# Kernel tuning notes

Measured on AMD Instinct MI355X. Metric: run time of the kernel, lower is better.

Reference implementation:

```python
import jax, jax.numpy as jnp
import numpy as np

B, N, C = 8, 4096, 3
IN_DIM = 2
HID = 512
NL = 256          # num_latents
DEPTH = 6
H, DH = 8, 64     # heads, dim_head (cross and latent)
INNER = H * DH
LAT = 32          # latent (bottleneck) dim
NF, MAXF = 12, 4  # NeRF num_freq, max_freq_log2
FF = 4 * HID
SCALE = DH ** -0.5
NERF_DIM = 2 * NF * IN_DIM  # 48


def layer_norm(x, g, b, eps=1e-5):
    m = jnp.mean(x, axis=-1, keepdims=True)
    v = jnp.mean((x - m) ** 2, axis=-1, keepdims=True)
    return (x - m) * jax.lax.rsqrt(v + eps) * g + b


def nerf_encode(pos):
    # log-sampled frequency bands: 2^linspace(0, MAXF, NF)
    freqs = 2.0 ** jnp.linspace(0.0, float(MAXF), NF)
    ang = pos[..., None] * freqs            # [B,N,IN_DIM,NF]
    enc = jnp.concatenate([jnp.sin(ang), jnp.cos(ang)], axis=-1)  # [B,N,IN_DIM,2NF]
    return enc.reshape(*pos.shape[:-1], NERF_DIM)


def mha(q, k, v):
    # q:[B,Nq,INNER] k,v:[B,Nk,INNER] -> [B,Nq,INNER]
    def split(t):
        b, n, _ = t.shape
        return t.reshape(b, n, H, DH).transpose(0, 2, 1, 3)  # [B,H,n,DH]
    qh, kh, vh = split(q), split(k), split(v)
    sim = jnp.einsum('bhid,bhjd->bhij', qh, kh) * SCALE
    attn = jax.nn.softmax(sim, axis=-1)
    o = jnp.einsum('bhij,bhjd->bhid', attn, vh)
    return o.transpose(0, 2, 1, 3).reshape(q.shape[0], q.shape[1], INNER)


def setup_inputs():
    key = jax.random.key(0)
    ks = iter(jax.random.split(key, 64))
    def w(*shape):
        return jax.random.normal(next(ks), shape, jnp.float32) * 0.02
    inp = {}
    inp['x'] = jax.random.normal(next(ks), (B, N, C), jnp.float32)
    inp['pos'] = jax.random.uniform(next(ks), (B, N, IN_DIM), jnp.float32)
    # input embeddings
    inp['W_pos'] = w(NERF_DIM, HID); inp['b_pos'] = jnp.zeros((HID,), jnp.float32)
    inp['W_in'] = w(C, HID); inp['b_in'] = jnp.zeros((HID,), jnp.float32)
    inp['latents'] = w(NL, HID)
    # cross-attention (PreNormCross: norm on q, k, v)
    for n in ('lnq', 'lnk', 'lnv'):
        inp[n + '_g'] = jnp.ones((HID,), jnp.float32)
        inp[n + '_b'] = jnp.zeros((HID,), jnp.float32)
    inp['cWq'] = w(HID, INNER); inp['cWk'] = w(HID, INNER); inp['cWv'] = w(HID, INNER)
    inp['cWo'] = w(INNER, HID); inp['c_bo'] = jnp.zeros((HID,), jnp.float32)
    # self-attention + FFN stacks
    inp['ln1_g'] = jnp.ones((DEPTH, HID), jnp.float32); inp['ln1_b'] = jnp.zeros((DEPTH, HID), jnp.float32)
    inp['sWq'] = w(DEPTH, HID, INNER); inp['sWkv'] = w(DEPTH, HID, 2 * INNER)
    inp['sWo'] = w(DEPTH, INNER, HID); inp['s_bo'] = jnp.zeros((DEPTH, HID), jnp.float32)
    inp['ln2_g'] = jnp.ones((DEPTH, HID), jnp.float32); inp['ln2_b'] = jnp.zeros((DEPTH, HID), jnp.float32)
    inp['fW1'] = w(DEPTH, HID, FF); inp['f_b1'] = jnp.zeros((DEPTH, FF), jnp.float32)
    inp['fW2'] = w(DEPTH, FF, HID); inp['f_b2'] = jnp.zeros((DEPTH, HID), jnp.float32)
    # final norm + gaussian bottleneck projection (mean, logvar)
    inp['lnf_g'] = jnp.ones((HID,), jnp.float32); inp['lnf_b'] = jnp.zeros((HID,), jnp.float32)
    inp['Wb'] = w(HID, 2 * LAT); inp['bb'] = jnp.zeros((2 * LAT,), jnp.float32)
    return inp


def reference(x, pos, W_pos, b_pos, W_in, b_in, latents,
              lnq_g, lnq_b, lnk_g, lnk_b, lnv_g, lnv_b,
              cWq, cWk, cWv, cWo, c_bo,
              ln1_g, ln1_b, sWq, sWkv, sWo, s_bo,
              ln2_g, ln2_b, fW1, f_b1, fW2, f_b2,
              lnf_g, lnf_b, Wb, bb):
    # positional embedding (FourierPositionalEmbedding with relu)
    kin = jax.nn.relu(nerf_encode(pos) @ W_pos + b_pos)   # [B,N,HID]
    vin = x @ W_in + b_in                                 # [B,N,HID]
    vin = vin + kin                                       # include_pos_in_value
    lat = jnp.broadcast_to(latents, (B, NL, HID))
    # cross-attention block (PreNormCross + residual)
    qn = layer_norm(lat, lnq_g, lnq_b)
    kn = layer_norm(kin, lnk_g, lnk_b)
    vn = layer_norm(vin, lnv_g, lnv_b)
    o = mha(qn @ cWq, kn @ cWk, vn @ cWv) @ cWo + c_bo
    lat = lat + o
    # latent self-attention + FFN blocks
    for i in range(DEPTH):
        h1 = layer_norm(lat, ln1_g[i], ln1_b[i])
        q = h1 @ sWq[i]
        k, v = jnp.split(h1 @ sWkv[i], 2, axis=-1)
        lat = lat + (mha(q, k, v) @ sWo[i] + s_bo[i])
        h2 = layer_norm(lat, ln2_g[i], ln2_b[i])
        lat = lat + (jax.nn.gelu(h2 @ fW1[i] + f_b1[i]) @ fW2[i] + f_b2[i])
    # bottleneck projection -> (mean | logvar)
    out = layer_norm(lat, lnf_g, lnf_b) @ Wb + bb         # [B,NL,2*LAT]
    return out
```

## Files before the change

### kernel.cpp

```cpp
#include <hip/hip_runtime.h>
#include <hip/hip_bf16.h>

#define DEV __device__ __forceinline__

typedef __attribute__((ext_vector_type(8))) short short8;
typedef __attribute__((ext_vector_type(4))) float floatx4;

DEV short f2bf(float f) {
  unsigned u = __float_as_uint(f);
  u += 0x7fffu + ((u >> 16) & 1u);
  return (short)(u >> 16);
}
DEV float bf2f(short s) {
  return __uint_as_float(((unsigned)(unsigned short)s) << 16);
}
DEV float wred(float v) {
#pragma unroll
  for (int m = 1; m < 64; m <<= 1) v += __shfl_xor(v, m);
  return v;
}
DEV floatx4 mfma16(short8 a, short8 b, floatx4 c) {
  return __builtin_amdgcn_mfma_f32_16x16x32_bf16(a, b, c, 0, 0, 0);
}
DEV void gload16(void* lds, const void* g) {
  __builtin_amdgcn_global_load_lds(
      (const __attribute__((address_space(1))) unsigned int*)g,
      (__attribute__((address_space(3))) unsigned int*)lds, 16, 0, 0);
}

struct MatDesc { const float* src; int K; int N; int kp; int off; };
struct MatTable { MatDesc m[36]; };

__global__ __launch_bounds__(256) void wtrans_kernel(MatTable T, short* __restrict__ dst) {
  int mi = blockIdx.y;
  MatDesc d = T.m[mi];
  int tilesx = d.N >> 5, tilesy = d.kp >> 5;
  int tb = blockIdx.x;
  if (tb >= tilesx * tilesy) return;
  int ty = tb / tilesx, tx = tb % tilesx;
  __shared__ float tile[32][33];
  int tid = threadIdx.x;
#pragma unroll
  for (int i = 0; i < 4; ++i) {
    int e = tid + i * 256, lr = e >> 5, lc = e & 31;
    int kk = ty * 32 + lr;
    tile[lr][lc] = (kk < d.K) ? d.src[(size_t)kk * d.N + tx * 32 + lc] : 0.f;
  }
  __syncthreads();
#pragma unroll
  for (int i = 0; i < 4; ++i) {
    int e = tid + i * 256, lr = e >> 5, lc = e & 31;
    dst[(size_t)d.off + (size_t)(tx * 32 + lr) * d.kp + ty * 32 + lc] = f2bf(tile[lc][lr]);
  }
}

__global__ __launch_bounds__(256) void enc_kernel(const float* __restrict__ pos,
                                                  short* __restrict__ enc) {
  int idx = blockIdx.x * 256 + threadIdx.x;
  int row = idx >> 3, oct = idx & 7;
  float p0 = pos[row * 2], p1 = pos[row * 2 + 1];
  short8 o;
#pragma unroll
  for (int j = 0; j < 8; ++j) {
    int k = oct * 8 + j;
    float val = 0.f;
    if (k < 48) {
      int dd = k / 24, rem = k % 24;
      int trig = rem / 12, f = rem % 12;
      float ang = (dd ? p1 : p0) * exp2f((4.0f / 11.0f) * (float)f);
      val = trig ? __cosf(ang) : __sinf(ang);
    }
    o[j] = f2bf(val);
  }
  *(short8*)&enc[(size_t)row * 64 + oct * 8] = o;
}

__global__ __launch_bounds__(512) void embed2_kernel(
    const short* __restrict__ enc, const short* __restrict__ Wt,
    const float* __restrict__ b_pos, const float* __restrict__ W_in,
    const float* __restrict__ b_in, const float* __restrict__ x,
    const float* __restrict__ lnk_g, const float* __restrict__ lnk_b,
    const float* __restrict__ lnv_g, const float* __restrict__ lnv_b,
    short* __restrict__ kn, short* __restrict__ vn) {
  __shared__ short Wl[512 * 64];
  __shared__ short El[128 * 64];
  int tid = threadIdx.x;
  int lane = tid & 63, wv = tid >> 6;
  int c = lane & 15, g = lane >> 4;
  int blk = blockIdx.x * 128;
#pragma unroll
  for (int gi = 0; gi < 8; ++gi) {
    int grp = wv * 8 + gi;
    int row = grp * 8 + (lane >> 3), kc = lane & 7;
    gload16(&Wl[grp * 512], &Wt[(size_t)row * 64 + ((kc ^ (row & 7)) * 8)]);
  }
#pragma unroll
  for (int gi = 0; gi < 2; ++gi) {
    int grp = wv * 2 + gi;
    int row = grp * 8 + (lane >> 3), kc = lane & 7;
    gload16(&El[grp * 512], &enc[(size_t)(blk + row) * 64 + ((kc ^ (row & 7)) * 8)]);
  }
  __syncthreads();

  floatx4 acc[32];
  floatx4 zf = {0.f, 0.f, 0.f, 0.f};
#pragma unroll
  for (int nf = 0; nf < 32; ++nf) acc[nf] = zf;
  short8 af[2];
#pragma unroll
  for (int ks = 0; ks < 2; ++ks)
    af[ks] = *(const short8*)&El[(wv * 16 + c) * 64 + ((ks * 4 + g) ^ (c & 7)) * 8];
#pragma unroll
  for (int nf = 0; nf < 32; ++nf) {
#pragma unroll
    for (int ks = 0; ks < 2; ++ks) {
      short8 bf8 = *(const short8*)&Wl[(nf * 16 + c) * 64 + ((ks * 4 + g) ^ (c & 7)) * 8];
      acc[nf] = mfma16(af[ks], bf8, acc[nf]);
    }
  }

  int rowbase = blk + wv * 16 + g * 4;
  float x0[4], x1[4], x2[4];
  float s1[4], q1[4], s2[4], q2[4];
#pragma unroll
  for (int r = 0; r < 4; ++r) {
    x0[r] = x[(size_t)(rowbase + r) * 3];
    x1[r] = x[(size_t)(rowbase + r) * 3 + 1];
    x2[r] = x[(size_t)(rowbase + r) * 3 + 2];
    s1[r] = 0; q1[r] = 0; s2[r] = 0; q2[r] = 0;
  }
#pragma unroll
  for (int nf = 0; nf < 32; ++nf) {
    int col = nf * 16 + c;
    float bp = b_pos[col];
    float w0 = W_in[col], w1 = W_in[512 + col], w2 = W_in[1024 + col], bi = b_in[col];
#pragma unroll
    for (int r = 0; r < 4; ++r) {
      float kk = fmaxf(acc[nf][r] + bp, 0.f);
      float vv = kk + x0[r] * w0 + x1[r] * w1 + x2[r] * w2 + bi;
      acc[nf][r] = kk;
      s1[r] += kk; q1[r] += kk * kk; s2[r] += vv; q2[r] += vv * vv;
    }
  }
  float m1[4], r1[4], m2[4], r2[4];
#pragma unroll
  for (int r = 0; r < 4; ++r) {
#pragma unroll
    for (int msk = 1; msk < 16; msk <<= 1) {
      s1[r] += __shfl_xor(s1[r], msk); q1[r] += __shfl_xor(q1[r], msk);
      s2[r] += __shfl_xor(s2[r], msk); q2[r] += __shfl_xor(q2[r], msk);
    }
    m1[r] = s1[r] * (1.f / 512.f);
    r1[r] = rsqrtf(q1[r] * (1.f / 512.f) - m1[r] * m1[r] + 1e-5f);
    m2[r] = s2[r] * (1.f / 512.f);
    r2[r] = rsqrtf(q2[r] * (1.f / 512.f) - m2[r] * m2[r] + 1e-5f);
  }
#pragma unroll
  for (int nf = 0; nf < 32; ++nf) {
    int col = nf * 16 + c;
    float w0 = W_in[col], w1 = W_in[512 + col], w2 = W_in[1024 + col], bi = b_in[col];
    float gk = lnk_g[col], bk = lnk_b[col], gv = lnv_g[col], bv = lnv_b[col];
#pragma unroll
    for (int r = 0; r < 4; ++r) {
      float kk = acc[nf][r];
      float vv = kk + x0[r] * w0 + x1[r] * w1 + x2[r] * w2 + bi;
      size_t idx = (size_t)(rowbase + r) * 512 + col;
      kn[idx] = f2bf((kk - m1[r]) * r1[r] * gk + bk);
      vn[idx] = f2bf((vv - m2[r]) * r2[r] * gv + bv);
    }
  }
}

__global__ __launch_bounds__(256) void ln_kernel(
    const float* __restrict__ in, const float* __restrict__ g,
    const float* __restrict__ b, short* __restrict__ out, int M) {
  int row = blockIdx.x * 4 + (threadIdx.x >> 6);
  if (row >= M) return;
  int lane = threadIdx.x & 63;
  float v[8]; float s = 0, q = 0;
#pragma unroll
  for (int j = 0; j < 8; ++j) {
    v[j] = in[(size_t)row * 512 + lane + 64 * j];
    s += v[j]; q += v[j] * v[j];
  }
  s = wred(s); q = wred(q);
  float m = s * (1.f / 512.f);
  float rs = rsqrtf(q * (1.f / 512.f) - m * m + 1e-5f);
#pragma unroll
  for (int j = 0; j < 8; ++j) {
    int cc = lane + 64 * j;
    out[(size_t)row * 512 + cc] = f2bf((v[j] - m) * rs * g[cc] + b[cc]);
  }
}

__global__ void bcast_kernel(const float* __restrict__ latents, float* __restrict__ lat) {
  int i = blockIdx.x * 256 + threadIdx.x;
  lat[i] = latents[i & 131071];
}

template <int EPI>
DEV void epi_store(void* outp, size_t idx, float xv) {
  if (EPI == 0) {
    ((short*)outp)[idx] = f2bf(xv);
  } else if (EPI == 1) {
    float t = 0.7978845608f * (xv + 0.044715f * xv * xv * xv);
    ((short*)outp)[idx] = f2bf(0.5f * xv * (1.f + tanhf(t)));
  } else if (EPI == 2) {
    ((float*)outp)[idx] += xv;
  } else {
    ((float*)outp)[idx] = xv;
  }
}

template <int EPI>
__global__ __launch_bounds__(256) void gemm_kernel(
    const short* __restrict__ A, const short* __restrict__ Wt,
    const float* __restrict__ bias, void* __restrict__ outp,
    int M, int N, int K, int ldo) {
  __shared__ short Alds[128 * 64];
  __shared__ short Blds[128 * 64];
  int tid = threadIdx.x;
  int brow = blockIdx.y * 128, bcol = blockIdx.x * 128;
  int lane = tid & 63, wvid = tid >> 6;
  int wr = wvid >> 1, wc = wvid & 1;
  int g = lane >> 4, c = lane & 15;
  floatx4 zf = {0.f, 0.f, 0.f, 0.f};
  floatx4 acc[4][4];
#pragma unroll
  for (int i = 0; i < 4; ++i)
#pragma unroll
    for (int j = 0; j < 4; ++j) acc[i][j] = zf;

  int srow = (lane >> 3), skc = lane & 7;
  for (int k0 = 0; k0 < K; k0 += 64) {
#pragma unroll
    for (int gi = 0; gi < 4; ++gi) {
      int grp = wvid * 4 + gi;
      int row = grp * 8 + srow;
      int sw = ((skc ^ (row & 7)) * 8);
      gload16(&Alds[grp * 512], &A[(size_t)(brow + row) * K + k0 + sw]);
      gload16(&Blds[grp * 512], &Wt[(size_t)(bcol + row) * K + k0 + sw]);
    }
    __syncthreads();
#pragma unroll
    for (int ks = 0; ks < 2; ++ks) {
      int slot = ((ks * 4 + g) ^ (c & 7)) * 8;
      short8 af[4], bf8[4];
#pragma unroll
      for (int mf = 0; mf < 4; ++mf)
        af[mf] = *(const short8*)&Alds[(wr * 64 + mf * 16 + c) * 64 + slot];
#pragma unroll
      for (int nf = 0; nf < 4; ++nf)
        bf8[nf] = *(const short8*)&Blds[(wc * 64 + nf * 16 + c) * 64 + slot];
#pragma unroll
      for (int mf = 0; mf < 4; ++mf)
#pragma unroll
        for (int nf = 0; nf < 4; ++nf)
          acc[mf][nf] = mfma16(af[mf], bf8[nf], acc[mf][nf]);
    }
    __syncthreads();
  }

#pragma unroll
  for (int mf = 0; mf < 4; ++mf) {
#pragma unroll
    for (int nf = 0; nf < 4; ++nf) {
      int col = bcol + wc * 64 + nf * 16 + c;
      float bv = bias ? bias[col] : 0.f;
      int row0 = brow + wr * 64 + mf * 16 + g * 4;
#pragma unroll
      for (int r = 0; r < 4; ++r)
        epi_store<EPI>(outp, (size_t)(row0 + r) * ldo + col, acc[mf][nf][r] + bv);
    }
  }
}

template <int EPI>
__global__ __launch_bounds__(256) void gemm64_kernel(
    const short* __restrict__ A, const short* __restrict__ Wt,
    const float* __restrict__ bias, void* __restrict__ outp,
    int M, int N, int K, int ldo) {
  __shared__ short Alds[64 * 64];
  __shared__ short Blds[64 * 64];
  int tid = threadIdx.x;
  int brow = blockIdx.y * 64, bcol = blockIdx.x * 64;
  int lane = tid & 63, wvid = tid >> 6;
  int wr = wvid >> 1, wc = wvid & 1;
  int g = lane >> 4, c = lane & 15;
  floatx4 zf = {0.f, 0.f, 0.f, 0.f};
  floatx4 acc[2][2];
#pragma unroll
  for (int i = 0; i < 2; ++i)
#pragma unroll
    for (int j = 0; j < 2; ++j) acc[i][j] = zf;

  int srow = (lane >> 3), skc = lane & 7;
  for (int k0 = 0; k0 < K; k0 += 64) {
#pragma unroll
    for (int gi = 0; gi < 2; ++gi) {
      int grp = wvid * 2 + gi;
      int row = grp * 8 + srow;
      int sw = ((skc ^ (row & 7)) * 8);
      gload16(&Alds[grp * 512], &A[(size_t)(brow + row) * K + k0 + sw]);
      gload16(&Blds[grp * 512], &Wt[(size_t)(bcol + row) * K + k0 + sw]);
    }
    __syncthreads();
#pragma unroll
    for (int ks = 0; ks < 2; ++ks) {
      int slot = ((ks * 4 + g) ^ (c & 7)) * 8;
      short8 af[2], bf8[2];
#pragma unroll
      for (int mf = 0; mf < 2; ++mf)
        af[mf] = *(const short8*)&Alds[(wr * 32 + mf * 16 + c) * 64 + slot];
#pragma unroll
      for (int nf = 0; nf < 2; ++nf)
        bf8[nf] = *(const short8*)&Blds[(wc * 32 + nf * 16 + c) * 64 + slot];
#pragma unroll
      for (int mf = 0; mf < 2; ++mf)
#pragma unroll
        for (int nf = 0; nf < 2; ++nf)
          acc[mf][nf] = mfma16(af[mf], bf8[nf], acc[mf][nf]);
    }
    __syncthreads();
  }

#pragma unroll
  for (int mf = 0; mf < 2; ++mf) {
#pragma unroll
    for (int nf = 0; nf < 2; ++nf) {
      int col = bcol + wc * 32 + nf * 16 + c;
      float bv = bias ? bias[col] : 0.f;
      int row0 = brow + wr * 32 + mf * 16 + g * 4;
#pragma unroll
      for (int r = 0; r < 4; ++r)
        epi_store<EPI>(outp, (size_t)(row0 + r) * ldo + col, acc[mf][nf][r] + bv);
    }
  }
}

__global__ __launch_bounds__(256) void flash_kernel(
    const short* __restrict__ q, const short* __restrict__ k,
    const short* __restrict__ v, short* __restrict__ out,
    int qrs, int qbrows, long kvbstride, int kvrstride, int nkv) {
  __shared__ short Qs[64 * 64];
  __shared__ short Ks[64 * 64];
  __shared__ short Vt[64 * 72];
  __shared__ short Ps[64 * 72];
  int tid = threadIdx.x;
  int b = blockIdx.z, h = blockIdx.y, qt = blockIdx.x;
  int lane = tid & 63, wv = tid >> 6;
  int g = lane >> 4, c = lane & 15;
  int srow = lane >> 3, skc = lane & 7;

#pragma unroll
  for (int gi = 0; gi < 2; ++gi) {
    int grp = wv * 2 + gi;
    int row = grp * 8 + srow;
    int sw = ((skc ^ (row & 7)) * 8);
    gload16(&Qs[grp * 512],
            &q[((size_t)(b * qbrows) + qt * 64 + row) * qrs + h * 64 + sw]);
  }

  float m_[4], l_[4];
  floatx4 zf = {0.f, 0.f, 0.f, 0.f};
  floatx4 o_[4];
#pragma unroll
  for (int r = 0; r < 4; ++r) { m_[r] = -3.0e38f; l_[r] = 0.f; }
#pragma unroll
  for (int f = 0; f < 4; ++f) o_[f] = zf;

  for (int t0 = 0; t0 < nkv; t0 += 64) {
#pragma unroll
    for (int gi = 0; gi < 2; ++gi) {
      int grp = wv * 2 + gi;
      int row = grp * 8 + srow;
      int sw = ((skc ^ (row & 7)) * 8);
      gload16(&Ks[grp * 512],
              &k[(size_t)b * kvbstride + (size_t)(t0 + row) * kvrstride + h * 64 + sw]);
    }
#pragma unroll
    for (int it = 0; it < 2; ++it) {
      int ch = tid + it * 256;
      int j = ch >> 3, f0 = (ch & 7) * 8, mm = ch & 7, tg = j >> 3;
      short8 tv = *(const short8*)&v[(size_t)b * kvbstride + (size_t)(t0 + j) * kvrstride + h * 64 + f0];
#pragma unroll
      for (int jj = 0; jj < 8; ++jj)
        Vt[(f0 + jj) * 72 + ((tg ^ mm) * 8) + (j & 7)] = tv[jj];
    }
    __syncthreads();

    floatx4 s[4];
#pragma unroll
    for (int f = 0; f < 4; ++f) s[f] = zf;
#pragma unroll
    for (int ks = 0; ks < 2; ++ks) {
      int slot = ((ks * 4 + g) ^ (c & 7)) * 8;
      short8 a = *(const short8*)&Qs[(wv * 16 + c) * 64 + slot];
#pragma unroll
      for (int f = 0; f < 4; ++f) {
        short8 b8 = *(const short8*)&Ks[(f * 16 + c) * 64 + slot];
        s[f] = mfma16(a, b8, s[f]);
      }
    }
#pragma unroll
    for (int f = 0; f < 4; ++f)
#pragma unroll
      for (int r = 0; r < 4; ++r) s[f][r] *= 0.125f;

    float nm[4], sf[4], rs[4];
#pragma unroll
    for (int r = 0; r < 4; ++r) {
      float t = fmaxf(fmaxf(s[0][r], s[1][r]), fmaxf(s[2][r], s[3][r]));
#pragma unroll
      for (int msk = 1; msk < 16; msk <<= 1) t = fmaxf(t, __shfl_xor(t, msk));
      nm[r] = fmaxf(m_[r], t);
      sf[r] = __expf(m_[r] - nm[r]);
      rs[r] = 0.f;
    }
#pragma unroll
    for (int f = 0; f < 4; ++f)
#pragma unroll
      for (int r = 0; r < 4; ++r) {
        float p = __expf(s[f][r] - nm[r]);
        s[f][r] = p; rs[r] += p;
      }
#pragma unroll
    for (int r = 0; r < 4; ++r) {
#pragma unroll
      for (int msk = 1; msk < 16; msk <<= 1) rs[r] += __shfl_xor(rs[r], msk);
      l_[r] = l_[r] * sf[r] + rs[r];
      m_[r] = nm[r];
    }
#pragma unroll
    for (int f = 0; f < 4; ++f)
#pragma unroll
      for (int r = 0; r < 4; ++r) o_[f][r] *= sf[r];
#pragma unroll
    for (int f = 0; f < 4; ++f)
#pragma unroll
      for (int r = 0; r < 4; ++r)
        Ps[(wv * 16 + g * 4 + r) * 72 + f * 16 + c] = f2bf(s[f][r]);
    __syncthreads();
#pragma unroll
    for (int ks = 0; ks < 2; ++ks) {
      short8 pa = *(const short8*)&Ps[(wv * 16 + c) * 72 + ks * 32 + g * 8];
#pragma unroll
      for (int f = 0; f < 4; ++f) {
        int mm = (2 * f + (c >> 3)) & 7;
        short8 vb = *(const short8*)&Vt[(f * 16 + c) * 72 + ((ks * 4 + g) ^ mm) * 8];
        o_[f] = mfma16(pa, vb, o_[f]);
      }
    }
    __syncthreads();
  }

#pragma unroll
  for (int f = 0; f < 4; ++f)
#pragma unroll
    for (int r = 0; r < 4; ++r) {
      int row = qt * 64 + wv * 16 + g * 4 + r;
      float val = o_[f][r] / l_[r];
      out[((size_t)(b * 256 + row)) * 512 + h * 64 + f * 16 + c] = f2bf(val);
    }
}

extern "C" void kernel_launch(void* const* d_in, const int* in_sizes, int n_in,
                              void* d_out, int out_size, void* d_ws, size_t ws_size,
                              hipStream_t stream) {
  const float* x       = (const float*)d_in[0];
  const float* pos     = (const float*)d_in[1];
  const float* W_pos   = (const float*)d_in[2];
  const float* b_pos   = (const float*)d_in[3];
  const float* W_in    = (const float*)d_in[4];
  const float* b_in    = (const float*)d_in[5];
  const float* latents = (const float*)d_in[6];
  const float* lnq_g   = (const float*)d_in[7];
  const float* lnq_b   = (const float*)d_in[8];
  const float* lnk_g   = (const float*)d_in[9];
  const float* lnk_b   = (const float*)d_in[10];
  const float* lnv_g   = (const float*)d_in[11];
  const float* lnv_b   = (const float*)d_in[12];
  const float* cWq     = (const float*)d_in[13];
  const float* cWk     = (const float*)d_in[14];
  const float* cWv     = (const float*)d_in[15];
  const float* cWo     = (const float*)d_in[16];
  const float* c_bo    = (const float*)d_in[17];
  const float* ln1_g   = (const float*)d_in[18];
  const float* ln1_b   = (const float*)d_in[19];
  const float* sWq     = (const float*)d_in[20];
  const float* sWkv    = (const float*)d_in[21];
  const float* sWo     = (const float*)d_in[22];
  const float* s_bo    = (const float*)d_in[23];
  const float* ln2_g   = (const float*)d_in[24];
  const float* ln2_b   = (const float*)d_in[25];
  const float* fW1     = (const float*)d_in[26];
  const float* f_b1    = (const float*)d_in[27];
  const float* fW2     = (const float*)d_in[28];
  const float* f_b2    = (const float*)d_in[29];
  const float* lnf_g   = (const float*)d_in[30];
  const float* lnf_b   = (const float*)d_in[31];
  const float* Wb      = (const float*)d_in[32];
  const float* bbv     = (const float*)d_in[33];
  float* outp = (float*)d_out;

  size_t W = 0;
  size_t o_cWq = W; W += 512 * 512;
  size_t o_cWk = W; W += 512 * 512;
  size_t o_cWv = W; W += 512 * 512;
  size_t o_cWo = W; W += 512 * 512;
  size_t o_Wb  = W; W += 64 * 512;
  size_t o_Wpos = W; W += 512 * 64;
  size_t o_sQKV[6], o_sWo[6], o_fW1[6], o_fW2[6];
  for (int i = 0; i < 6; ++i) {
    o_sQKV[i] = W; W += 1536 * 512;
    o_sWo[i]  = W; W += 512 * 512;
    o_fW1[i]  = W; W += 2048 * 512;
    o_fW2[i]  = W; W += 512 * 2048;
  }
  MatTable T;
  int nm = 0;
  auto add = [&](const float* s, int K, int N, int kp, size_t off) {
    T.m[nm].src = s; T.m[nm].K = K; T.m[nm].N = N; T.m[nm].kp = kp;
    T.m[nm].off = (int)off; ++nm;
  };
  add(cWq, 512, 512, 512, o_cWq); add(cWk, 512, 512, 512, o_cWk);
  add(cWv, 512, 512, 512, o_cWv); add(cWo, 512, 512, 512, o_cWo);
  add(Wb, 512, 64, 512, o_Wb);
  add(W_pos, 48, 512, 64, o_Wpos);
  for (int i = 0; i < 6; ++i) {
    add(sWq  + (size_t)i * 512 * 512,  512, 512,  512, o_sQKV[i]);
    add(sWkv + (size_t)i * 512 * 1024, 512, 1024, 512, o_sQKV[i] + 512 * 512);
    add(sWo  + (size_t)i * 512 * 512,  512, 512,  512, o_sWo[i]);
    add(fW1  + (size_t)i * 512 * 2048, 512, 2048, 512, o_fW1[i]);
    add(fW2  + (size_t)i * 2048 * 512, 2048, 512, 2048, o_fW2[i]);
  }

  char* p = (char*)d_ws;
  auto carve = [&](size_t bytes) {
    char* r = p; p += (bytes + 255) & ~(size_t)255; return r;
  };
  short* wtb   = (short*)carve(W * 2);
  short* enc   = (short*)carve((size_t)32768 * 64 * 2);
  short* kn    = (short*)carve(33554432);
  short* vn    = (short*)carve(33554432);
  short* kvc   = (short*)carve((size_t)32768 * 1024 * 2);
  short* latn0 = (short*)carve(262144);
  short* qc    = (short*)carve(262144);
  float* lat   = (float*)carve(4194304);
  short* attno = kn;
  short* h     = vn;
  short* qkv   = (short*)((char*)vn + 2097152);
  short* ffh   = (short*)((char*)vn + 8388608);

  wtrans_kernel<<<dim3(1024, 36), 256, 0, stream>>>(T, wtb);
  enc_kernel<<<1024, 256, 0, stream>>>(pos, enc);
  embed2_kernel<<<256, 512, 0, stream>>>(enc, wtb + o_Wpos, b_pos, W_in, b_in, x,
                                         lnk_g, lnk_b, lnv_g, lnv_b, kn, vn);
  bcast_kernel<<<4096, 256, 0, stream>>>(latents, lat);
  ln_kernel<<<64, 256, 0, stream>>>(latents, lnq_g, lnq_b, latn0, 256);
  gemm64_kernel<0><<<dim3(8, 4), 256, 0, stream>>>(latn0, wtb + o_cWq, nullptr, qc, 256, 512, 512, 512);
  gemm_kernel<0><<<dim3(4, 256), 256, 0, stream>>>(kn, wtb + o_cWk, nullptr, kvc, 32768, 512, 512, 1024);
  gemm_kernel<0><<<dim3(4, 256), 256, 0, stream>>>(vn, wtb + o_cWv, nullptr, kvc + 512, 32768, 512, 512, 1024);
  flash_kernel<<<dim3(4, 8, 8), 256, 0, stream>>>(qc, kvc, kvc + 512, attno,
                                                  512, 0, (long)4096 * 1024, 1024, 4096);
  gemm64_kernel<2><<<dim3(8, 32), 256, 0, stream>>>(attno, wtb + o_cWo, c_bo, lat, 2048, 512, 512, 512);

  for (int i = 0; i < 6; ++i) {
    ln_kernel<<<512, 256, 0, stream>>>(lat, ln1_g + i * 512, ln1_b + i * 512, h, 2048);
    gemm64_kernel<0><<<dim3(24, 32), 256, 0, stream>>>(h, wtb + o_sQKV[i], nullptr, qkv, 2048, 1536, 512, 1536);
    flash_kernel<<<dim3(4, 8, 8), 256, 0, stream>>>(qkv, qkv + 512, qkv + 1024, attno,
                                                    1536, 256, (long)256 * 1536, 1536, 256);
    gemm64_kernel<2><<<dim3(8, 32), 256, 0, stream>>>(attno, wtb + o_sWo[i], s_bo + i * 512, lat, 2048, 512, 512, 512);
    ln_kernel<<<512, 256, 0, stream>>>(lat, ln2_g + i * 512, ln2_b + i * 512, h, 2048);
    gemm_kernel<1><<<dim3(16, 16), 256, 0, stream>>>(h, wtb + o_fW1[i], f_b1 + i * 2048, ffh, 2048, 2048, 512, 2048);
    gemm64_kernel<2><<<dim3(8, 32), 256, 0, stream>>>(ffh, wtb + o_fW2[i], f_b2 + i * 512, lat, 2048, 512, 2048, 512);
  }
  ln_kernel<<<512, 256, 0, stream>>>(lat, lnf_g, lnf_b, h, 2048);
  gemm64_kernel<3><<<dim3(1, 32), 256, 0, stream>>>(h, wtb + o_Wb, bbv, outp, 2048, 64, 512, 64);
}
```

Measured before the change: 888.8 us.

## Split attention over KV segments with a combine kernel; interleave kn/vn buffers

Replaces the single-pass flash attention with a split-KV variant that writes per-segment partial outputs, row maxima and sums, followed by a combine kernel that rescales and merges them. Cross-attention uses 8 segments and self-attention uses 2, raising grid size from 256 blocks to 2048/512 so more CUs are occupied. Also interleaves kn/vn into one row-strided buffer (adding an lda parameter to the GEMMs) and switches the FFN up-projection to the 64-tile GEMM. The cost is extra fp32 partial traffic and an additional kernel launch per attention.

```diff
diff --git a/kernel.cpp b/kernel.cpp
--- a/kernel.cpp
+++ b/kernel.cpp
@@ -81,7 +81,7 @@
     const float* __restrict__ b_in, const float* __restrict__ x,
     const float* __restrict__ lnk_g, const float* __restrict__ lnk_b,
     const float* __restrict__ lnv_g, const float* __restrict__ lnv_b,
-    short* __restrict__ kn, short* __restrict__ vn) {
+    short* __restrict__ knvn) {
   __shared__ short Wl[512 * 64];
   __shared__ short El[128 * 64];
   int tid = threadIdx.x;
@@ -164,9 +164,9 @@
     for (int r = 0; r < 4; ++r) {
       float kk = acc[nf][r];
       float vv = kk + x0[r] * w0 + x1[r] * w1 + x2[r] * w2 + bi;
-      size_t idx = (size_t)(rowbase + r) * 512 + col;
-      kn[idx] = f2bf((kk - m1[r]) * r1[r] * gk + bk);
-      vn[idx] = f2bf((vv - m2[r]) * r2[r] * gv + bv);
+      size_t ridx = (size_t)(rowbase + r) * 1024;
+      knvn[ridx + col] = f2bf((kk - m1[r]) * r1[r] * gk + bk);
+      knvn[ridx + 512 + col] = f2bf((vv - m2[r]) * r2[r] * gv + bv);
     }
   }
 }
@@ -216,7 +216,7 @@
 __global__ __launch_bounds__(256) void gemm_kernel(
     const short* __restrict__ A, const short* __restrict__ Wt,
     const float* __restrict__ bias, void* __restrict__ outp,
-    int M, int N, int K, int ldo) {
+    int M, int N, int K, int lda, int ldo) {
   __shared__ short Alds[128 * 64];
   __shared__ short Blds[128 * 64];
   int tid = threadIdx.x;
@@ -238,7 +238,7 @@
       int grp = wvid * 4 + gi;
       int row = grp * 8 + srow;
       int sw = ((skc ^ (row & 7)) * 8);
-      gload16(&Alds[grp * 512], &A[(size_t)(brow + row) * K + k0 + sw]);
+      gload16(&Alds[grp * 512], &A[(size_t)(brow + row) * lda + k0 + sw]);
       gload16(&Blds[grp * 512], &Wt[(size_t)(bcol + row) * K + k0 + sw]);
     }
     __syncthreads();
@@ -279,7 +279,7 @@
 __global__ __launch_bounds__(256) void gemm64_kernel(
     const short* __restrict__ A, const short* __restrict__ Wt,
     const float* __restrict__ bias, void* __restrict__ outp,
-    int M, int N, int K, int ldo) {
+    int M, int N, int K, int lda, int ldo) {
   __shared__ short Alds[64 * 64];
   __shared__ short Blds[64 * 64];
   int tid = threadIdx.x;
@@ -301,7 +301,7 @@
       int grp = wvid * 2 + gi;
       int row = grp * 8 + srow;
       int sw = ((skc ^ (row & 7)) * 8);
-      gload16(&Alds[grp * 512], &A[(size_t)(brow + row) * K + k0 + sw]);
+      gload16(&Alds[grp * 512], &A[(size_t)(brow + row) * lda + k0 + sw]);
       gload16(&Blds[grp * 512], &Wt[(size_t)(bcol + row) * K + k0 + sw]);
     }
     __syncthreads();
@@ -338,16 +338,20 @@
   }
 }
 
-__global__ __launch_bounds__(256) void flash_kernel(
+__global__ __launch_bounds__(256) void flashsp_kernel(
     const short* __restrict__ q, const short* __restrict__ k,
-    const short* __restrict__ v, short* __restrict__ out,
-    int qrs, int qbrows, long kvbstride, int kvrstride, int nkv) {
+    const short* __restrict__ v, float* __restrict__ po,
+    float* __restrict__ pm, float* __restrict__ pl,
+    int qrs, int qbrows, long kvbstride, int kvrstride,
+    int seglen, int lognseg) {
   __shared__ short Qs[64 * 64];
   __shared__ short Ks[64 * 64];
   __shared__ short Vt[64 * 72];
   __shared__ short Ps[64 * 72];
   int tid = threadIdx.x;
-  int b = blockIdx.z, h = blockIdx.y, qt = blockIdx.x;
+  int bz = blockIdx.z;
+  int b = bz >> lognseg, seg = bz & ((1 << lognseg) - 1);
+  int h = blockIdx.y, qt = blockIdx.x;
   int lane = tid & 63, wv = tid >> 6;
   int g = lane >> 4, c = lane & 15;
   int srow = lane >> 3, skc = lane & 7;
@@ -369,7 +373,8 @@
 #pragma unroll
   for (int f = 0; f < 4; ++f) o_[f] = zf;
 
-  for (int t0 = 0; t0 < nkv; t0 += 64) {
+  int tbeg = seg * seglen, tend = tbeg + seglen;
+  for (int t0 = tbeg; t0 < tend; t0 += 64) {
 #pragma unroll
     for (int gi = 0; gi < 2; ++gi) {
       int grp = wv * 2 + gi;
@@ -459,9 +464,36 @@
 #pragma unroll
     for (int r = 0; r < 4; ++r) {
       int row = qt * 64 + wv * 16 + g * 4 + r;
-      float val = o_[f][r] / l_[r];
-      out[((size_t)(b * 256 + row)) * 512 + h * 64 + f * 16 + c] = f2bf(val);
-    }
+      size_t grow = (size_t)seg * 2048 + b * 256 + row;
+      po[grow * 512 + h * 64 + f * 16 + c] = o_[f][r];
+      if (f == 0 && c == 0) {
+        pm[grow * 8 + h] = m_[r];
+        pl[grow * 8 + h] = l_[r];
+      }
+    }
+}
+
+template <int NSEG>
+__global__ __launch_bounds__(256) void fcomb_kernel(
+    const float* __restrict__ po, const float* __restrict__ pm,
+    const float* __restrict__ pl, short* __restrict__ out) {
+  int idx = blockIdx.x * 256 + threadIdx.x;
+  int grow = idx >> 9, col = idx & 511, h = col >> 6;
+  float ms[NSEG];
+  float M = -3.0e38f;
+#pragma unroll
+  for (int s = 0; s < NSEG; ++s) {
+    ms[s] = pm[((size_t)s * 2048 + grow) * 8 + h];
+    M = fmaxf(M, ms[s]);
+  }
+  float L = 0.f, acc = 0.f;
+#pragma unroll
+  for (int s = 0; s < NSEG; ++s) {
+    float w = __expf(ms[s] - M);
+    L += w * pl[((size_t)s * 2048 + grow) * 8 + h];
+    acc += w * po[((size_t)s * 2048 + grow) * 512 + col];
+  }
+  out[idx] = f2bf(acc / L);
 }
 
 extern "C" void kernel_launch(void* const* d_in, const int* in_sizes, int n_in,
@@ -541,40 +573,44 @@
   };
   short* wtb   = (short*)carve(W * 2);
   short* enc   = (short*)carve((size_t)32768 * 64 * 2);
-  short* kn    = (short*)carve(33554432);
-  short* vn    = (short*)carve(33554432);
+  short* knvn  = (short*)carve((size_t)32768 * 1024 * 2);
   short* kvc   = (short*)carve((size_t)32768 * 1024 * 2);
   short* latn0 = (short*)carve(262144);
   short* qc    = (short*)carve(262144);
   float* lat   = (float*)carve(4194304);
-  short* attno = kn;
-  short* h     = vn;
-  short* qkv   = (short*)((char*)vn + 2097152);
-  short* ffh   = (short*)((char*)vn + 8388608);
+  float* pm    = (float*)carve(1048576);
+  float* pl    = (float*)carve(1048576);
+  short* attno = enc;
+  float* po    = (float*)knvn;
+  short* h     = (short*)((char*)knvn + 36 * 1048576);
+  short* qkv   = (short*)((char*)knvn + 40 * 1048576);
+  short* ffh   = (short*)((char*)knvn + 48 * 1048576);
 
   wtrans_kernel<<<dim3(1024, 36), 256, 0, stream>>>(T, wtb);
   enc_kernel<<<1024, 256, 0, stream>>>(pos, enc);
   embed2_kernel<<<256, 512, 0, stream>>>(enc, wtb + o_Wpos, b_pos, W_in, b_in, x,
-                                         lnk_g, lnk_b, lnv_g, lnv_b, kn, vn);
+                                         lnk_g, lnk_b, lnv_g, lnv_b, knvn);
   bcast_kernel<<<4096, 256, 0, stream>>>(latents, lat);
   ln_kernel<<<64, 256, 0, stream>>>(latents, lnq_g, lnq_b, latn0, 256);
-  gemm64_kernel<0><<<dim3(8, 4), 256, 0, stream>>>(latn0, wtb + o_cWq, nullptr, qc, 256, 512, 512, 512);
-  gemm_kernel<0><<<dim3(4, 256), 256, 0, stream>>>(kn, wtb + o_cWk, nullptr, kvc, 32768, 512, 512, 1024);
-  gemm_kernel<0><<<dim3(4, 256), 256, 0, stream>>>(vn, wtb + o_cWv, nullptr, kvc + 512, 32768, 512, 512, 1024);
-  flash_kernel<<<dim3(4, 8, 8), 256, 0, stream>>>(qc, kvc, kvc + 512, attno,
-                                                  512, 0, (long)4096 * 1024, 1024, 4096);
-  gemm64_kernel<2><<<dim3(8, 32), 256, 0, stream>>>(attno, wtb + o_cWo, c_bo, lat, 2048, 512, 512, 512);
+  gemm64_kernel<0><<<dim3(8, 4), 256, 0, stream>>>(latn0, wtb + o_cWq, nullptr, qc, 256, 512, 512, 512, 512);
+  gemm_kernel<0><<<dim3(4, 256), 256, 0, stream>>>(knvn, wtb + o_cWk, nullptr, kvc, 32768, 512, 512, 1024, 1024);
+  gemm_kernel<0><<<dim3(4, 256), 256, 0, stream>>>(knvn + 512, wtb + o_cWv, nullptr, kvc + 512, 32768, 512, 512, 1024, 1024);
+  flashsp_kernel<<<dim3(4, 8, 64), 256, 0, stream>>>(qc, kvc, kvc + 512, po, pm, pl,
+                                                     512, 0, (long)4096 * 1024, 1024, 512, 3);
+  fcomb_kernel<8><<<4096, 256, 0, stream>>>(po, pm, pl, attno);
+  gemm64_kernel<2><<<dim3(8, 32), 256, 0, stream>>>(attno, wtb + o_cWo, c_bo, lat, 2048, 512, 512, 512, 512);
 
   for (int i = 0; i < 6; ++i) {
     ln_kernel<<<512, 256, 0, stream>>>(lat, ln1_g + i * 512, ln1_b + i * 512, h, 2048);
-    gemm64_kernel<0><<<dim3(24, 32), 256, 0, stream>>>(h, wtb + o_sQKV[i], nullptr, qkv, 2048, 1536, 512, 1536);
-    flash_kernel<<<dim3(4, 8, 8), 256, 0, stream>>>(qkv, qkv + 512, qkv + 1024, attno,
-                                                    1536, 256, (long)256 * 1536, 1536, 256);
-    gemm64_kernel<2><<<dim3(8, 32), 256, 0, stream>>>(attno, wtb + o_sWo[i], s_bo + i * 512, lat, 2048, 512, 512, 512);
+    gemm64_kernel<0><<<dim3(24, 32), 256, 0, stream>>>(h, wtb + o_sQKV[i], nullptr, qkv, 2048, 1536, 512, 512, 1536);
+    flashsp_kernel<<<dim3(4, 8, 16), 256, 0, stream>>>(qkv, qkv + 512, qkv + 1024, po, pm, pl,
+                                                       1536, 256, (long)256 * 1536, 1536, 128, 1);
+    fcomb_kernel<2><<<4096, 256, 0, stream>>>(po, pm, pl, attno);
+    gemm64_kernel<2><<<dim3(8, 32), 256, 0, stream>>>(attno, wtb + o_sWo[i], s_bo + i * 512, lat, 2048, 512, 512, 512, 512);
     ln_kernel<<<512, 256, 0, stream>>>(lat, ln2_g + i * 512, ln2_b + i * 512, h, 2048);
-    gemm_kernel<1><<<dim3(16, 16), 256, 0, stream>>>(h, wtb + o_fW1[i], f_b1 + i * 2048, ffh, 2048, 2048, 512, 2048);
-    gemm64_kernel<2><<<dim3(8, 32), 256, 0, stream>>>(ffh, wtb + o_fW2[i], f_b2 + i * 512, lat, 2048, 512, 2048, 512);
+    gemm64_kernel<1><<<dim3(32, 32), 256, 0, stream>>>(h, wtb + o_fW1[i], f_b1 + i * 2048, ffh, 2048, 2048, 512, 512, 2048);
+    gemm64_kernel<2><<<dim3(8, 32), 256, 0, stream>>>(ffh, wtb + o_fW2[i], f_b2 + i * 512, lat, 2048, 512, 2048, 2048, 512);
   }
   ln_kernel<<<512, 256, 0, stream>>>(lat, lnf_g, lnf_b, h, 2048);
-  gemm64_kernel<3><<<dim3(1, 32), 256, 0, stream>>>(h, wtb + o_Wb, bbv, outp, 2048, 64, 512, 64);
-}
+  gemm64_kernel<3><<<dim3(1, 32), 256, 0, stream>>>(h, wtb + o_Wb, bbv, outp, 2048, 64, 512, 512, 64);
+}
```

Measured after the change: 798.9 us. 1.11x faster.
